# Optimization experiments

Measured on AMD Instinct MI355X. Metric: run time of the kernel, lower is better.

The kernel has to match this reference:

```python
import jax, jax.numpy as jnp
import numpy as np

RATIO = 0.08  # self.ratio_3 (frozen parameter)
# kernel point k -> (dx, dy) = (k//3-1, k%3-1); matches torch.meshgrid('ij') flattening in offset_modulation
GX = np.repeat(np.arange(-1, 2), 3)  # [-1,-1,-1,0,0,0,1,1,1]
GY = np.tile(np.arange(-1, 2), 3)    # [-1,0,1,-1,0,1,-1,0,1]


def conv3(x, w, b):
    y = jax.lax.conv_general_dilated(x, w, (1, 1), ((1, 1), (1, 1)),
                                     dimension_numbers=('NCHW', 'OIHW', 'NCHW'))
    return y + b[None, :, None, None]


def offset_modulation(offset):
    B, C, H, W = offset.shape
    ov = offset.reshape(B, C // 2, 2, H, W)
    crop = ov[:, 3:12]                      # 9 (x,y) pairs
    oxy = jnp.concatenate([crop[:, :, 0], crop[:, :, 1]], axis=1) * RATIO  # [B,18,H,W]
    grid = jnp.concatenate([jnp.asarray(GX), jnp.asarray(GY)]).astype(offset.dtype)
    return oxy - grid[None, :, None, None]


def bilinear_sample(x, py, px):
    # x: [B,C,H,W]; py,px: [B,H,W] float sample coords; zero outside bounds
    B, C, H, W = x.shape
    y0 = jnp.floor(py); x0 = jnp.floor(px)
    wy = py - y0; wx = px - x0
    def gather(yi, xi):
        valid = ((yi >= 0) & (yi < H) & (xi >= 0) & (xi < W)).astype(x.dtype)
        yc = jnp.clip(yi, 0, H - 1).astype(jnp.int32)
        xc = jnp.clip(xi, 0, W - 1).astype(jnp.int32)
        g = jax.vmap(lambda img, yy, xx: img[:, yy, xx])(x, yc, xc)  # [B,C,H,W]
        return g * valid[:, None]
    return (gather(y0, x0) * ((1 - wy) * (1 - wx))[:, None]
            + gather(y0, x0 + 1) * ((1 - wy) * wx)[:, None]
            + gather(y0 + 1, x0) * (wy * (1 - wx))[:, None]
            + gather(y0 + 1, x0 + 1) * (wy * wx)[:, None])


def deform_conv(x, off, w, b):
    # off: [B,18,H,W], channels 0..8 = dx per kernel point, 9..17 = dy
    B, C, H, W = x.shape
    by = jnp.arange(H, dtype=x.dtype)[None, :, None]
    bx = jnp.arange(W, dtype=x.dtype)[None, None, :]
    out = jnp.zeros((B, w.shape[0], H, W), x.dtype)
    for k in range(9):
        py = by + GY[k] + off[:, 9 + k]
        px = bx + GX[k] + off[:, k]
        s = bilinear_sample(x, py, px)
        out = out + jnp.einsum('bchw,oc->bohw', s, w[:, :, GY[k] + 1, GX[k] + 1])
    return out + b[None, :, None, None]


def setup_inputs():
    key = jax.random.key(0)
    ks = iter(jax.random.split(key, 32))
    def p(*shape):
        return jax.random.normal(next(ks), shape, jnp.float32) * 0.05
    inp = {
        'x': jax.random.normal(next(ks), (2, 64, 256, 256), jnp.float32),
        'offset_0': jax.random.normal(next(ks), (2, 24, 256, 256), jnp.float32),
        'l12_w': p(64, 64, 3, 3), 'l12_b': p(64),
        'l13_w1': p(64, 64, 3, 3), 'l13_b1': p(64),
        'l13_w2': p(64, 64, 3, 3), 'l13_b2': p(64),
        'l14_w1': p(64, 64, 3, 3), 'l14_b1': p(64),
        'l14_w2': p(64, 64, 3, 3), 'l14_b2': p(64),
        'l15_w': p(32, 64, 3, 3), 'l15_b': p(32),
        'd50_w': p(32, 32, 3, 3), 'd50_b': p(32),
        'd51_w': p(32, 32, 3, 3), 'd51_b': p(32),
        'd60_w': p(32, 32, 3, 3), 'd60_b': p(32),
        'd61_w': p(32, 32, 3, 3), 'd61_b': p(32),
        'l24_w': p(3, 32, 3, 3), 'l24_b': p(3),
    }
    return inp


def reference(x, offset_0, l12_w, l12_b, l13_w1, l13_b1, l13_w2, l13_b2,
              l14_w1, l14_b1, l14_w2, l14_b2, l15_w, l15_b,
              d50_w, d50_b, d51_w, d51_b, d60_w, d60_b, d61_w, d61_b,
              l24_w, l24_b):
    off = offset_modulation(offset_0)
    x = conv3(x, l12_w, l12_b)
    x = conv3(jax.nn.relu(conv3(x, l13_w1, l13_b1)), l13_w2, l13_b2) + x
    x = conv3(jax.nn.relu(conv3(x, l14_w1, l14_b1)), l14_w2, l14_b2) + x
    x = conv3(x, l15_w, l15_b)
    r5 = jax.nn.relu(deform_conv(x, off, d50_w, d50_b))
    r5 = deform_conv(r5, off, d51_w, d51_b)
    x = x + r5
    r6 = jax.nn.relu(deform_conv(x, off, d60_w, d60_b))
    r6 = deform_conv(r6, off, d61_w, d61_b)
    x = x + r6
    return conv3(x, l24_w, l24_b)
```

## Files before the change

### kernel.cpp

```cpp
#include <hip/hip_runtime.h>

#define HH 256
#define WW 256
#define HW (HH * WW)

typedef float f32x4 __attribute__((ext_vector_type(4)));
typedef short bf16x8 __attribute__((ext_vector_type(8)));

__device__ __forceinline__ unsigned short f2bf(float f) {
    union { float f; unsigned u; } v; v.f = f;
    unsigned r = v.u + 0x7fff + ((v.u >> 16) & 1);
    return (unsigned short)(r >> 16);
}
__device__ __forceinline__ float bflo(unsigned u) {
    union { unsigned u; float f; } v; v.u = u << 16; return v.f;
}
__device__ __forceinline__ float bfhi(unsigned u) {
    union { unsigned u; float f; } v; v.u = u & 0xffff0000u; return v.f;
}

__global__ void prepack_all(
    const float* w0, const float* w1, const float* w2, const float* w3,
    const float* w4, const float* w5, const float* w6, const float* w7,
    const float* w8, const float* w9,
    unsigned short* d0, unsigned short* d1, unsigned short* d2,
    unsigned short* d3, unsigned short* d4, unsigned short* d5,
    unsigned short* d6, unsigned short* d7, unsigned short* d8,
    unsigned short* d9) {
    const int L = blockIdx.y;
    const float* w; unsigned short* dst; int COUT, CIN;
    switch (L) {
        case 0: w = w0; dst = d0; COUT = 64; CIN = 64; break;
        case 1: w = w1; dst = d1; COUT = 64; CIN = 64; break;
        case 2: w = w2; dst = d2; COUT = 64; CIN = 64; break;
        case 3: w = w3; dst = d3; COUT = 64; CIN = 64; break;
        case 4: w = w4; dst = d4; COUT = 64; CIN = 64; break;
        case 5: w = w5; dst = d5; COUT = 32; CIN = 64; break;
        case 6: w = w6; dst = d6; COUT = 32; CIN = 32; break;
        case 7: w = w7; dst = d7; COUT = 32; CIN = 32; break;
        case 8: w = w8; dst = d8; COUT = 32; CIN = 32; break;
        default: w = w9; dst = d9; COUT = 32; CIN = 32; break;
    }
    int n = COUT * CIN * 9;
    int i = blockIdx.x * 256 + threadIdx.x;
    if (i >= n) return;
    int q = i & 31;
    int rest = i >> 5;
    int o = rest % COUT;
    int rest2 = rest / COUT;
    int KC = CIN >> 5;
    int kc = rest2 % KC;
    int t = rest2 / KC;
    int cin = kc * 32 + q;
    float v = w[((o * CIN + cin) * 3 + t / 3) * 3 + (t % 3)];
    dst[i] = f2bf(v);
}

template <bool SRCF32, int CIN, int COUT, bool RELU, bool ADDRES>
__global__ __launch_bounds__(256) void convmfma(
    const void* __restrict__ in_, const unsigned short* __restrict__ wp,
    const float* __restrict__ bias, const unsigned short* __restrict__ res,
    unsigned short* __restrict__ out) {
    constexpr int KC = CIN / 32;
    constexpr int WM = COUT / 16;
    constexpr int CSTR = 72;
    __shared__ unsigned short xt[340 * CSTR];

    const int tid = threadIdx.x;
    const int b = blockIdx.z;
    const int bx0 = blockIdx.x * 32;
    const int by0 = blockIdx.y * 8;

    if (SRCF32) {
        const float* inb = (const float*)in_ + (size_t)b * CIN * HW;
        for (int hp = tid; hp < 340; hp += 256) {
            int hy = hp / 34, hx = hp - hy * 34;
            int gy = by0 + hy - 1, gx = bx0 + hx - 1;
            bool ok = ((unsigned)gy < HH) && ((unsigned)gx < WW);
            const float* src = inb + ((size_t)gy * WW + gx);
            unsigned* dstp = (unsigned*)&xt[hp * CSTR];
#pragma unroll 4
            for (int c = 0; c < CIN; c += 2) {
                float v0 = ok ? src[(size_t)c * HW] : 0.f;
                float v1 = ok ? src[(size_t)(c + 1) * HW] : 0.f;
                dstp[c >> 1] = (unsigned)f2bf(v0) | ((unsigned)f2bf(v1) << 16);
            }
        }
    } else {
        const unsigned short* inb = (const unsigned short*)in_ + (size_t)b * HW * CIN;
        constexpr int CH = CIN / 8;
        for (int idx = tid; idx < 340 * CH; idx += 256) {
            int hp = idx / CH, sub = idx - hp * CH;
            int hy = hp / 34, hx = hp - hy * 34;
            int gy = by0 + hy - 1, gx = bx0 + hx - 1;
            uint4 v = {0, 0, 0, 0};
            if (((unsigned)gy < HH) && ((unsigned)gx < WW))
                v = *(const uint4*)&inb[((size_t)gy * WW + gx) * CIN + sub * 8];
            *(uint4*)&xt[hp * CSTR + sub * 8] = v;
        }
    }
    __syncthreads();

    const int lane = tid & 63;
    const int wv = tid >> 6;
    const int l15 = lane & 15;
    const int kg = lane >> 4;

    f32x4 acc[WM][4];
#pragma unroll
    for (int m = 0; m < WM; ++m)
#pragma unroll
        for (int n = 0; n < 4; ++n) acc[m][n] = {0.f, 0.f, 0.f, 0.f};

    int hbase[4];
#pragma unroll
    for (int n = 0; n < 4; ++n) {
        int p = n * 16 + l15;
        hbase[n] = (2 * wv + (p >> 5)) * 34 + (p & 31);
    }

    const unsigned short* wlane = wp + ((size_t)l15 * 4 + kg) * 8;

#pragma unroll
    for (int t = 0; t < 9; ++t) {
        bf16x8 afr[WM][KC];
#pragma unroll
        for (int kc = 0; kc < KC; ++kc)
#pragma unroll
            for (int m = 0; m < WM; ++m)
                afr[m][kc] = *(const bf16x8*)(wlane + ((size_t)(t * KC + kc) * COUT + m * 16) * 32);

        const int hoff = (t / 3) * 34 + (t % 3);
#pragma unroll
        for (int kc = 0; kc < KC; ++kc) {
            bf16x8 bfr[4];
#pragma unroll
            for (int n = 0; n < 4; ++n)
                bfr[n] = *(const bf16x8*)&xt[(hbase[n] + hoff) * CSTR + kc * 32 + kg * 8];
#pragma unroll
            for (int m = 0; m < WM; ++m)
#pragma unroll
                for (int n = 0; n < 4; ++n)
                    acc[m][n] = __builtin_amdgcn_mfma_f32_16x16x32_bf16(afr[m][kc], bfr[n], acc[m][n], 0, 0, 0);
        }
    }

    const size_t pixbase = (size_t)b * HW;
#pragma unroll
    for (int n = 0; n < 4; ++n) {
        int p = n * 16 + l15;
        int gy = by0 + 2 * wv + (p >> 5), gx = bx0 + (p & 31);
        size_t pidx = (pixbase + (size_t)gy * WW + gx) * COUT;
#pragma unroll
        for (int m = 0; m < WM; ++m) {
            int cb = m * 16 + kg * 4;
            float v[4];
#pragma unroll
            for (int r = 0; r < 4; ++r) {
                v[r] = acc[m][n][r] + bias[cb + r];
                if (RELU) v[r] = fmaxf(v[r], 0.f);
            }
            if (ADDRES) {
                uint2 rr = *(const uint2*)&res[pidx + cb];
                v[0] += bflo(rr.x); v[1] += bfhi(rr.x);
                v[2] += bflo(rr.y); v[3] += bfhi(rr.y);
            }
            uint2 o;
            o.x = (unsigned)f2bf(v[0]) | ((unsigned)f2bf(v[1]) << 16);
            o.y = (unsigned)f2bf(v[2]) | ((unsigned)f2bf(v[3]) << 16);
            *(uint2*)&out[pidx + cb] = o;
        }
    }
}

__global__ __launch_bounds__(512) void dpair(
    const unsigned short* __restrict__ in, const float* __restrict__ off0,
    const unsigned short* __restrict__ w1p, const float* __restrict__ b1,
    const unsigned short* __restrict__ w2p, const float* __restrict__ b2,
    unsigned short* __restrict__ out) {
    constexpr int CS = 40;
    constexpr int MIDB = 432 * CS;
    __shared__ unsigned short xt[(432 + 352) * CS];

    const int tid = threadIdx.x;
    const int b = blockIdx.z;
    const int bx0 = blockIdx.x * 32;
    const int by0 = blockIdx.y * 8;

    const unsigned short* inb = in + (size_t)b * HW * 32;
    for (int idx = tid; idx < 432 * 4; idx += 512) {
        int hp = idx >> 2, sub = idx & 3;
        int hy = hp / 36, hx = hp - hy * 36;
        int gy = by0 + hy - 2, gx = bx0 + hx - 2;
        uint4 v = {0, 0, 0, 0};
        if (((unsigned)gy < HH) && ((unsigned)gx < WW))
            v = *(const uint4*)&inb[((size_t)gy * WW + gx) * 32 + sub * 8];
        *(uint4*)&xt[hp * CS + sub * 8] = v;
    }
    __syncthreads();

    const int lane = tid & 63;
    const int wv = tid >> 6;
    const int l15 = lane & 15;
    const int kg = lane >> 4;
    const float* offB = off0 + (size_t)b * 24 * HW;

    f32x4 acc1[2][3];
#pragma unroll
    for (int m = 0; m < 2; ++m)
#pragma unroll
        for (int f = 0; f < 3; ++f) acc1[m][f] = {0.f, 0.f, 0.f, 0.f};

    int fgy[3], fgx[3], foff[3];
#pragma unroll
    for (int f = 0; f < 3; ++f) {
        int id = (wv * 3 + f) * 16 + l15;
        int rid = min(id, 339);
        int iy = rid / 34, ix = rid - iy * 34;
        fgy[f] = by0 - 1 + iy;
        fgx[f] = bx0 - 1 + ix;
        int cy = min(max(fgy[f], 0), HH - 1);
        int cx = min(max(fgx[f], 0), WW - 1);
        foff[f] = cy * WW + cx;
    }
    const unsigned short* w1l = w1p + (size_t)(l15 * 32 + kg * 8);

#pragma unroll 1
    for (int t = 0; t < 9; ++t) {
        const int k = (t % 3) * 3 + t / 3;
        const float* offx = offB + (size_t)(6 + 2 * k) * HW;
        const float* offy = offB + (size_t)(7 + 2 * k) * HW;
        bf16x8 afr[2];
#pragma unroll
        for (int m = 0; m < 2; ++m)
            afr[m] = *(const bf16x8*)(w1l + (size_t)(t * 32 + m * 16) * 32);

        bf16x8 bfr[3];
#pragma unroll
        for (int f = 0; f < 3; ++f) {
            float dxv = offx[foff[f]] * 0.08f;
            float dyv = offy[foff[f]] * 0.08f;
            float pxf = (float)fgx[f] + dxv;
            float pyf = (float)fgy[f] + dyv;
            float x0f = floorf(pxf), y0f = floorf(pyf);
            float wx = pxf - x0f, wy = pyf - y0f;
            int tx0 = min(max((int)x0f - (bx0 - 2), 0), 34);
            int ty0 = min(max((int)y0f - (by0 - 2), 0), 10);
            int lp = ty0 * 36 + tx0;
            uint4 a00 = *(const uint4*)&xt[lp * CS + kg * 8];
            uint4 a01 = *(const uint4*)&xt[(lp + 1) * CS + kg * 8];
            uint4 a10 = *(const uint4*)&xt[(lp + 36) * CS + kg * 8];
            uint4 a11 = *(const uint4*)&xt[(lp + 37) * CS + kg * 8];
            float w00 = (1.f - wy) * (1.f - wx), w01 = (1.f - wy) * wx;
            float w10 = wy * (1.f - wx), w11 = wy * wx;
            unsigned c00[4] = {a00.x, a00.y, a00.z, a00.w};
            unsigned c01[4] = {a01.x, a01.y, a01.z, a01.w};
            unsigned c10[4] = {a10.x, a10.y, a10.z, a10.w};
            unsigned c11[4] = {a11.x, a11.y, a11.z, a11.w};
            union { bf16x8 v; unsigned u[4]; } ur;
#pragma unroll
            for (int j = 0; j < 4; ++j) {
                float slo = w00 * bflo(c00[j]) + w01 * bflo(c01[j]) +
                            w10 * bflo(c10[j]) + w11 * bflo(c11[j]);
                float shi = w00 * bfhi(c00[j]) + w01 * bfhi(c01[j]) +
                            w10 * bfhi(c10[j]) + w11 * bfhi(c11[j]);
                ur.u[j] = (unsigned)f2bf(slo) | ((unsigned)f2bf(shi) << 16);
            }
            bfr[f] = ur.v;
        }
#pragma unroll
        for (int m = 0; m < 2; ++m)
#pragma unroll
            for (int f = 0; f < 3; ++f)
                acc1[m][f] = __builtin_amdgcn_mfma_f32_16x16x32_bf16(afr[m], bfr[f], acc1[m][f], 0, 0, 0);
    }
#pragma unroll
    for (int f = 0; f < 3; ++f) {
        int id = (wv * 3 + f) * 16 + l15;
        bool ok = ((unsigned)fgy[f] < HH) && ((unsigned)fgx[f] < WW) && (id < 340);
        int wid = min(id, 351);
#pragma unroll
        for (int m = 0; m < 2; ++m) {
            int cb = m * 16 + kg * 4;
            float v[4];
#pragma unroll
            for (int r = 0; r < 4; ++r)
                v[r] = ok ? fmaxf(acc1[m][f][r] + b1[cb + r], 0.f) : 0.f;
            uint2 o;
            o.x = (unsigned)f2bf(v[0]) | ((unsigned)f2bf(v[1]) << 16);
            o.y = (unsigned)f2bf(v[2]) | ((unsigned)f2bf(v[3]) << 16);
            *(uint2*)&xt[MIDB + wid * CS + cb] = o;
        }
    }
    __syncthreads();

    f32x4 acc2[2][2];
#pragma unroll
    for (int m = 0; m < 2; ++m)
#pragma unroll
        for (int n = 0; n < 2; ++n) acc2[m][n] = {0.f, 0.f, 0.f, 0.f};

    const int py = by0 + wv;
    const unsigned short* w2l = w2p + (size_t)(l15 * 32 + kg * 8);

#pragma unroll 1
    for (int t = 0; t < 9; ++t) {
        const int k = (t % 3) * 3 + t / 3;
        const float* offx = offB + (size_t)(6 + 2 * k) * HW + (size_t)py * WW;
        const float* offy = offB + (size_t)(7 + 2 * k) * HW + (size_t)py * WW;
        bf16x8 afr[2];
#pragma unroll
        for (int m = 0; m < 2; ++m)
            afr[m] = *(const bf16x8*)(w2l + (size_t)(t * 32 + m * 16) * 32);

        bf16x8 bfr[2];
#pragma unroll
        for (int n = 0; n < 2; ++n) {
            const int pxi = bx0 + n * 16 + l15;
            float dxv = offx[pxi] * 0.08f;
            float dyv = offy[pxi] * 0.08f;
            float pxf = (float)pxi + dxv;
            float pyf = (float)py + dyv;
            float x0f = floorf(pxf), y0f = floorf(pyf);
            float wx = pxf - x0f, wy = pyf - y0f;
            int mx0 = min(max((int)x0f - (bx0 - 1), 0), 32);
            int my0 = min(max((int)y0f - (by0 - 1), 0), 8);
            int lp = my0 * 34 + mx0;
            uint4 a00 = *(const uint4*)&xt[MIDB + lp * CS + kg * 8];
            uint4 a01 = *(const uint4*)&xt[MIDB + (lp + 1) * CS + kg * 8];
            uint4 a10 = *(const uint4*)&xt[MIDB + (lp + 34) * CS + kg * 8];
            uint4 a11 = *(const uint4*)&xt[MIDB + (lp + 35) * CS + kg * 8];
            float w00 = (1.f - wy) * (1.f - wx), w01 = (1.f - wy) * wx;
            float w10 = wy * (1.f - wx), w11 = wy * wx;
            unsigned c00[4] = {a00.x, a00.y, a00.z, a00.w};
            unsigned c01[4] = {a01.x, a01.y, a01.z, a01.w};
            unsigned c10[4] = {a10.x, a10.y, a10.z, a10.w};
            unsigned c11[4] = {a11.x, a11.y, a11.z, a11.w};
            union { bf16x8 v; unsigned u[4]; } ur;
#pragma unroll
            for (int j = 0; j < 4; ++j) {
                float slo = w00 * bflo(c00[j]) + w01 * bflo(c01[j]) +
                            w10 * bflo(c10[j]) + w11 * bflo(c11[j]);
                float shi = w00 * bfhi(c00[j]) + w01 * bfhi(c01[j]) +
                            w10 * bfhi(c10[j]) + w11 * bfhi(c11[j]);
                ur.u[j] = (unsigned)f2bf(slo) | ((unsigned)f2bf(shi) << 16);
            }
            bfr[n] = ur.v;
        }
#pragma unroll
        for (int m = 0; m < 2; ++m)
#pragma unroll
            for (int n = 0; n < 2; ++n)
                acc2[m][n] = __builtin_amdgcn_mfma_f32_16x16x32_bf16(afr[m], bfr[n], acc2[m][n], 0, 0, 0);
    }

    unsigned short* outb = out + (size_t)b * HW * 32;
#pragma unroll
    for (int n = 0; n < 2; ++n) {
        int gx = bx0 + n * 16 + l15;
        int rs = (wv + 2) * 36 + (n * 16 + l15) + 2;
        size_t pidx = ((size_t)py * WW + gx) * 32;
#pragma unroll
        for (int m = 0; m < 2; ++m) {
            int cb = m * 16 + kg * 4;
            float v[4];
#pragma unroll
            for (int r = 0; r < 4; ++r) v[r] = acc2[m][n][r] + b2[cb + r];
            uint2 rr = *(const uint2*)&xt[rs * CS + cb];
            v[0] += bflo(rr.x); v[1] += bfhi(rr.x);
            v[2] += bflo(rr.y); v[3] += bfhi(rr.y);
            uint2 o;
            o.x = (unsigned)f2bf(v[0]) | ((unsigned)f2bf(v[1]) << 16);
            o.y = (unsigned)f2bf(v[2]) | ((unsigned)f2bf(v[3]) << 16);
            *(uint2*)&outb[pidx + cb] = o;
        }
    }
}

__global__ __launch_bounds__(256) void conv3f(const unsigned short* __restrict__ in,
                                              const float* __restrict__ wgt,
                                              const float* __restrict__ bias,
                                              float* __restrict__ out) {
    __shared__ unsigned short xt[324 * 34];
    const int tid = threadIdx.x;
    const int lx = tid & 15, ly = tid >> 4;
    const int bx = blockIdx.x << 4, by = blockIdx.y << 4;
    const int b = blockIdx.z;

    const unsigned short* inb = in + (size_t)b * HW * 32;
    for (int idx = tid; idx < 324 * 8; idx += 256) {
        int hp = idx >> 3, sub = idx & 7;
        int hy = hp / 18, hx = hp - hy * 18;
        int gy = by + hy - 1, gx = bx + hx - 1;
        uint2 v = {0, 0};
        if (((unsigned)gy < HH) && ((unsigned)gx < WW))
            v = *(const uint2*)&inb[((size_t)gy * WW + gx) * 32 + sub * 4];
        *(uint2*)&xt[hp * 34 + sub * 4] = v;
    }
    __syncthreads();

    float a0 = bias[0], a1 = bias[1], a2 = bias[2];
#pragma unroll
    for (int ty = 0; ty < 3; ++ty) {
#pragma unroll
        for (int tx = 0; tx < 3; ++tx) {
            const unsigned short* row = &xt[((ly + ty) * 18 + lx + tx) * 34];
#pragma unroll 8
            for (int c = 0; c < 32; c += 2) {
                unsigned pv = *(const unsigned*)&row[c];
                float vl = bflo(pv), vh = bfhi(pv);
                const float* wl = wgt + (size_t)(c * 3 + ty) * 3 + tx;
                const float* whp = wgt + (size_t)((c + 1) * 3 + ty) * 3 + tx;
                a0 = fmaf(vl, wl[0], a0);          a0 = fmaf(vh, whp[0], a0);
                a1 = fmaf(vl, wl[32 * 9], a1);     a1 = fmaf(vh, whp[32 * 9], a1);
                a2 = fmaf(vl, wl[64 * 9], a2);     a2 = fmaf(vh, whp[64 * 9], a2);
            }
        }
    }
    const size_t o0 = ((size_t)b * 3) * HW + (size_t)(by + ly) * WW + bx + lx;
    out[o0] = a0;
    out[o0 + HW] = a1;
    out[o0 + 2 * HW] = a2;
}

extern "C" void kernel_launch(void* const* d_in, const int* in_sizes, int n_in,
                              void* d_out, int out_size, void* d_ws, size_t ws_size,
                              hipStream_t stream) {
    const float* x    = (const float*)d_in[0];
    const float* off0 = (const float*)d_in[1];
    const float* w12  = (const float*)d_in[2];
    const float* b12  = (const float*)d_in[3];
    const float* w13a = (const float*)d_in[4];
    const float* b13a = (const float*)d_in[5];
    const float* w13b = (const float*)d_in[6];
    const float* b13b = (const float*)d_in[7];
    const float* w14a = (const float*)d_in[8];
    const float* b14a = (const float*)d_in[9];
    const float* w14b = (const float*)d_in[10];
    const float* b14b = (const float*)d_in[11];
    const float* w15  = (const float*)d_in[12];
    const float* b15  = (const float*)d_in[13];
    const float* w50  = (const float*)d_in[14];
    const float* b50  = (const float*)d_in[15];
    const float* w51  = (const float*)d_in[16];
    const float* b51  = (const float*)d_in[17];
    const float* w60  = (const float*)d_in[18];
    const float* b60  = (const float*)d_in[19];
    const float* w61  = (const float*)d_in[20];
    const float* b61  = (const float*)d_in[21];
    const float* w24  = (const float*)d_in[22];
    const float* b24  = (const float*)d_in[23];

    unsigned short* A  = (unsigned short*)d_ws;
    unsigned short* Bb = A + (size_t)2 * HW * 64;
    unsigned short* D  = Bb;
    unsigned short* E  = Bb + (size_t)2 * HW * 32;
    unsigned short* wpk = Bb + (size_t)2 * HW * 64;
    const int SZ64 = 64 * 64 * 9;
    const int SZ32 = 32 * 64 * 9;
    const int SZD  = 32 * 32 * 9;
    unsigned short* p12  = wpk;
    unsigned short* p13a = p12 + SZ64;
    unsigned short* p13b = p13a + SZ64;
    unsigned short* p14a = p13b + SZ64;
    unsigned short* p14b = p14a + SZ64;
    unsigned short* p15  = p14b + SZ64;
    unsigned short* q50  = p15 + SZ32;
    unsigned short* q51  = q50 + SZD;
    unsigned short* q60  = q51 + SZD;
    unsigned short* q61  = q60 + SZD;
    float* out = (float*)d_out;

    prepack_all<<<dim3(144, 10), 256, 0, stream>>>(
        w12, w13a, w13b, w14a, w14b, w15, w50, w51, w60, w61,
        p12, p13a, p13b, p14a, p14b, p15, q50, q51, q60, q61);

    dim3 gm(WW / 32, HH / 8, 2);
    dim3 gd(WW / 32, HH / 8, 2);
    dim3 gs(HH / 16, WW / 16, 2);

    convmfma<true,  64, 64, false, false><<<gm, 256, 0, stream>>>(x,  p12,  b12,  nullptr, A);
    convmfma<false, 64, 64, true,  false><<<gm, 256, 0, stream>>>(A,  p13a, b13a, nullptr, Bb);
    convmfma<false, 64, 64, false, true ><<<gm, 256, 0, stream>>>(Bb, p13b, b13b, A, A);
    convmfma<false, 64, 64, true,  false><<<gm, 256, 0, stream>>>(A,  p14a, b14a, nullptr, Bb);
    convmfma<false, 64, 64, false, true ><<<gm, 256, 0, stream>>>(Bb, p14b, b14b, A, A);
    convmfma<false, 64, 32, false, false><<<gm, 256, 0, stream>>>(A,  p15,  b15,  nullptr, D);

    dpair<<<gd, 512, 0, stream>>>(D, off0, q50, b50, q51, b51, E);
    dpair<<<gd, 512, 0, stream>>>(E, off0, q60, b60, q61, b61, D);
    conv3f<<<gs, 256, 0, stream>>>(D, w24, b24, out);
}
```

Baseline: 254.6 us.

## Shrink conv tiles to 4 rows, split waves over channels, use packed bf16 cvt

The MFMA conv kernel now covers a 32x4 pixel tile per block instead of 32x8. The waves are split over both output-channel halves and pixel groups, and the 64->32 layer launches with 128 threads. The grid doubles, raising occupancy and shrinking shared memory per block, at the cost of more halo reloading relative to useful work. Separately, bf16 packing switches to the hardware v_cvt_pk_bf16_f32 instruction, and the bilinear sums in the deformable kernel use explicit fmaf chains.

```diff
diff --git a/kernel.cpp b/kernel.cpp
--- a/kernel.cpp
+++ b/kernel.cpp
@@ -17,6 +17,11 @@
 }
 __device__ __forceinline__ float bfhi(unsigned u) {
     union { unsigned u; float f; } v; v.u = u & 0xffff0000u; return v.f;
+}
+__device__ __forceinline__ unsigned cvtpk(float lo, float hi) {
+    unsigned r;
+    asm("v_cvt_pk_bf16_f32 %0, %1, %2" : "=v"(r) : "v"(lo), "v"(hi));
+    return r;
 }
 
 __global__ void prepack_all(
@@ -57,23 +62,24 @@
 }
 
 template <bool SRCF32, int CIN, int COUT, bool RELU, bool ADDRES>
-__global__ __launch_bounds__(256) void convmfma(
+__global__ __launch_bounds__((COUT / 32) * 128) void convmfma(
     const void* __restrict__ in_, const unsigned short* __restrict__ wp,
     const float* __restrict__ bias, const unsigned short* __restrict__ res,
     unsigned short* __restrict__ out) {
     constexpr int KC = CIN / 32;
-    constexpr int WM = COUT / 16;
-    constexpr int CSTR = 72;
-    __shared__ unsigned short xt[340 * CSTR];
+    constexpr int WM = COUT / 32;
+    constexpr int NT = WM * 128;
+    constexpr int CSTR = (CIN == 64) ? 72 : 40;
+    __shared__ unsigned short xt[204 * CSTR];
 
     const int tid = threadIdx.x;
     const int b = blockIdx.z;
     const int bx0 = blockIdx.x * 32;
-    const int by0 = blockIdx.y * 8;
+    const int by0 = blockIdx.y * 4;
 
     if (SRCF32) {
         const float* inb = (const float*)in_ + (size_t)b * CIN * HW;
-        for (int hp = tid; hp < 340; hp += 256) {
+        for (int hp = tid; hp < 204; hp += NT) {
             int hy = hp / 34, hx = hp - hy * 34;
             int gy = by0 + hy - 1, gx = bx0 + hx - 1;
             bool ok = ((unsigned)gy < HH) && ((unsigned)gx < WW);
@@ -83,13 +89,13 @@
             for (int c = 0; c < CIN; c += 2) {
                 float v0 = ok ? src[(size_t)c * HW] : 0.f;
                 float v1 = ok ? src[(size_t)(c + 1) * HW] : 0.f;
-                dstp[c >> 1] = (unsigned)f2bf(v0) | ((unsigned)f2bf(v1) << 16);
+                dstp[c >> 1] = cvtpk(v0, v1);
             }
         }
     } else {
         const unsigned short* inb = (const unsigned short*)in_ + (size_t)b * HW * CIN;
         constexpr int CH = CIN / 8;
-        for (int idx = tid; idx < 340 * CH; idx += 256) {
+        for (int idx = tid; idx < 204 * CH; idx += NT) {
             int hp = idx / CH, sub = idx - hp * CH;
             int hy = hp / 34, hx = hp - hy * 34;
             int gy = by0 + hy - 1, gx = bx0 + hx - 1;
@@ -103,31 +109,33 @@
 
     const int lane = tid & 63;
     const int wv = tid >> 6;
+    const int wm = (WM == 2) ? (wv & 1) : 0;
+    const int wn = (WM == 2) ? (wv >> 1) : wv;
     const int l15 = lane & 15;
     const int kg = lane >> 4;
 
-    f32x4 acc[WM][4];
-#pragma unroll
-    for (int m = 0; m < WM; ++m)
+    f32x4 acc[2][4];
+#pragma unroll
+    for (int m = 0; m < 2; ++m)
 #pragma unroll
         for (int n = 0; n < 4; ++n) acc[m][n] = {0.f, 0.f, 0.f, 0.f};
 
     int hbase[4];
 #pragma unroll
     for (int n = 0; n < 4; ++n) {
-        int p = n * 16 + l15;
-        hbase[n] = (2 * wv + (p >> 5)) * 34 + (p & 31);
-    }
-
-    const unsigned short* wlane = wp + ((size_t)l15 * 4 + kg) * 8;
+        int p = wn * 64 + n * 16 + l15;
+        hbase[n] = (p >> 5) * 34 + (p & 31);
+    }
+
+    const unsigned short* wlane = wp + ((size_t)(wm * 32 + l15) * 4 + kg) * 8;
 
 #pragma unroll
     for (int t = 0; t < 9; ++t) {
-        bf16x8 afr[WM][KC];
+        bf16x8 afr[2][KC];
 #pragma unroll
         for (int kc = 0; kc < KC; ++kc)
 #pragma unroll
-            for (int m = 0; m < WM; ++m)
+            for (int m = 0; m < 2; ++m)
                 afr[m][kc] = *(const bf16x8*)(wlane + ((size_t)(t * KC + kc) * COUT + m * 16) * 32);
 
         const int hoff = (t / 3) * 34 + (t % 3);
@@ -138,7 +146,7 @@
             for (int n = 0; n < 4; ++n)
                 bfr[n] = *(const bf16x8*)&xt[(hbase[n] + hoff) * CSTR + kc * 32 + kg * 8];
 #pragma unroll
-            for (int m = 0; m < WM; ++m)
+            for (int m = 0; m < 2; ++m)
 #pragma unroll
                 for (int n = 0; n < 4; ++n)
                     acc[m][n] = __builtin_amdgcn_mfma_f32_16x16x32_bf16(afr[m][kc], bfr[n], acc[m][n], 0, 0, 0);
@@ -147,13 +155,13 @@
 
     const size_t pixbase = (size_t)b * HW;
 #pragma unroll
-    for (int n = 0; n < 4; ++n) {
-        int p = n * 16 + l15;
-        int gy = by0 + 2 * wv + (p >> 5), gx = bx0 + (p & 31);
-        size_t pidx = (pixbase + (size_t)gy * WW + gx) * COUT;
-#pragma unroll
-        for (int m = 0; m < WM; ++m) {
-            int cb = m * 16 + kg * 4;
+    for (int m = 0; m < 2; ++m) {
+#pragma unroll
+        for (int n = 0; n < 4; ++n) {
+            int p = wn * 64 + n * 16 + l15;
+            int gy = by0 + (p >> 5), gx = bx0 + (p & 31);
+            size_t pidx = (pixbase + (size_t)gy * WW + gx) * COUT;
+            int cb = wm * 32 + m * 16 + kg * 4;
             float v[4];
 #pragma unroll
             for (int r = 0; r < 4; ++r) {
@@ -166,8 +174,8 @@
                 v[2] += bflo(rr.y); v[3] += bfhi(rr.y);
             }
             uint2 o;
-            o.x = (unsigned)f2bf(v[0]) | ((unsigned)f2bf(v[1]) << 16);
-            o.y = (unsigned)f2bf(v[2]) | ((unsigned)f2bf(v[3]) << 16);
+            o.x = cvtpk(v[0], v[1]);
+            o.y = cvtpk(v[2], v[3]);
             *(uint2*)&out[pidx + cb] = o;
         }
     }
@@ -260,11 +268,15 @@
             union { bf16x8 v; unsigned u[4]; } ur;
 #pragma unroll
             for (int j = 0; j < 4; ++j) {
-                float slo = w00 * bflo(c00[j]) + w01 * bflo(c01[j]) +
-                            w10 * bflo(c10[j]) + w11 * bflo(c11[j]);
-                float shi = w00 * bfhi(c00[j]) + w01 * bfhi(c01[j]) +
-                            w10 * bfhi(c10[j]) + w11 * bfhi(c11[j]);
-                ur.u[j] = (unsigned)f2bf(slo) | ((unsigned)f2bf(shi) << 16);
+                float slo = w00 * bflo(c00[j]);
+                slo = fmaf(w01, bflo(c01[j]), slo);
+                slo = fmaf(w10, bflo(c10[j]), slo);
+                slo = fmaf(w11, bflo(c11[j]), slo);
+                float shi = w00 * bfhi(c00[j]);
+                shi = fmaf(w01, bfhi(c01[j]), shi);
+                shi = fmaf(w10, bfhi(c10[j]), shi);
+                shi = fmaf(w11, bfhi(c11[j]), shi);
+                ur.u[j] = cvtpk(slo, shi);
             }
             bfr[f] = ur.v;
         }
@@ -287,8 +299,8 @@
             for (int r = 0; r < 4; ++r)
                 v[r] = ok ? fmaxf(acc1[m][f][r] + b1[cb + r], 0.f) : 0.f;
             uint2 o;
-            o.x = (unsigned)f2bf(v[0]) | ((unsigned)f2bf(v[1]) << 16);
-            o.y = (unsigned)f2bf(v[2]) | ((unsigned)f2bf(v[3]) << 16);
+            o.x = cvtpk(v[0], v[1]);
+            o.y = cvtpk(v[2], v[3]);
             *(uint2*)&xt[MIDB + wid * CS + cb] = o;
         }
     }
@@ -339,11 +351,15 @@
             union { bf16x8 v; unsigned u[4]; } ur;
 #pragma unroll
             for (int j = 0; j < 4; ++j) {
-                float slo = w00 * bflo(c00[j]) + w01 * bflo(c01[j]) +
-                            w10 * bflo(c10[j]) + w11 * bflo(c11[j]);
-                float shi = w00 * bfhi(c00[j]) + w01 * bfhi(c01[j]) +
-                            w10 * bfhi(c10[j]) + w11 * bfhi(c11[j]);
-                ur.u[j] = (unsigned)f2bf(slo) | ((unsigned)f2bf(shi) << 16);
+                float slo = w00 * bflo(c00[j]);
+                slo = fmaf(w01, bflo(c01[j]), slo);
+                slo = fmaf(w10, bflo(c10[j]), slo);
+                slo = fmaf(w11, bflo(c11[j]), slo);
+                float shi = w00 * bfhi(c00[j]);
+                shi = fmaf(w01, bfhi(c01[j]), shi);
+                shi = fmaf(w10, bfhi(c10[j]), shi);
+                shi = fmaf(w11, bfhi(c11[j]), shi);
+                ur.u[j] = cvtpk(slo, shi);
             }
             bfr[n] = ur.v;
         }
@@ -370,8 +386,8 @@
             v[0] += bflo(rr.x); v[1] += bfhi(rr.x);
             v[2] += bflo(rr.y); v[3] += bfhi(rr.y);
             uint2 o;
-            o.x = (unsigned)f2bf(v[0]) | ((unsigned)f2bf(v[1]) << 16);
-            o.y = (unsigned)f2bf(v[2]) | ((unsigned)f2bf(v[3]) << 16);
+            o.x = cvtpk(v[0], v[1]);
+            o.y = cvtpk(v[2], v[3]);
             *(uint2*)&outb[pidx + cb] = o;
         }
     }
@@ -475,7 +491,7 @@
         w12, w13a, w13b, w14a, w14b, w15, w50, w51, w60, w61,
         p12, p13a, p13b, p14a, p14b, p15, q50, q51, q60, q61);
 
-    dim3 gm(WW / 32, HH / 8, 2);
+    dim3 gm(WW / 32, HH / 4, 2);
     dim3 gd(WW / 32, HH / 8, 2);
     dim3 gs(HH / 16, WW / 16, 2);
 
@@ -484,7 +500,7 @@
     convmfma<false, 64, 64, false, true ><<<gm, 256, 0, stream>>>(Bb, p13b, b13b, A, A);
     convmfma<false, 64, 64, true,  false><<<gm, 256, 0, stream>>>(A,  p14a, b14a, nullptr, Bb);
     convmfma<false, 64, 64, false, true ><<<gm, 256, 0, stream>>>(Bb, p14b, b14b, A, A);
-    convmfma<false, 64, 32, false, false><<<gm, 256, 0, stream>>>(A,  p15,  b15,  nullptr, D);
+    convmfma<false, 64, 32, false, false><<<gm, 128, 0, stream>>>(A,  p15,  b15,  nullptr, D);
 
     dpair<<<gd, 512, 0, stream>>>(D, off0, q50, b50, q51, b51, E);
     dpair<<<gd, 512, 0, stream>>>(E, off0, q60, b60, q61, b61, D);
```

New measurement: 217.2 us. 14.7% less time.
